# Kernel tuning notes

Hardware: AMD Instinct MI355X
Metric: run time of the kernel (lower is better)

The kernel has to match this reference:

```python
import jax, jax.numpy as jnp
import numpy as np

V, E, L, T, H, B = 8124, 1024, 24, 512, 16, 2
S = E // H
DFF = E * 8 // 3  # 2730
EPS = 1e-5
SCALE = 1.0 / np.sqrt(E)  # note: 1/sqrt(emb_dim), as in the source


def _pe():
    # sinusoidal positional encoding [T, E]
    pos = jnp.arange(T, dtype=jnp.float32)[:, None]
    div = jnp.exp(jnp.arange(0, E, 2, dtype=jnp.float32) * (-np.log(10000.0) / E))
    pe = jnp.zeros((T, E), jnp.float32)
    pe = pe.at[:, 0::2].set(jnp.sin(pos * div))
    pe = pe.at[:, 1::2].set(jnp.cos(pos * div))
    return pe


def _rms(x, g):
    # NOTE: source takes the mean over the WHOLE tensor (no dim arg)
    rms = jnp.sqrt(jnp.mean(x.astype(jnp.float32) ** 2) + EPS)
    return (x / rms * g).astype(x.dtype)


def setup_inputs() -> dict:
    key = jax.random.key(0)
    ks = jax.random.split(key, 9)
    def w(k, shape):
        return jax.random.normal(k, shape, jnp.float32) * 0.02
    return {
        "tokens": jax.random.randint(ks[0], (B, T), 0, V),
        "emb_table": w(ks[1], (V, E)),
        "Wqkv": w(ks[2], (L, E, 3 * E)), "bqkv": jnp.zeros((L, 3 * E), jnp.float32),
        "Wo": w(ks[3], (L, E, E)), "bo": jnp.zeros((L, E), jnp.float32),
        "W1": w(ks[4], (L, E, DFF)), "b1": jnp.zeros((L, DFF), jnp.float32),
        "W3": w(ks[5], (L, E, DFF)), "b3": jnp.zeros((L, DFF), jnp.float32),
        "W2": w(ks[6], (L, DFF, E)), "b2": jnp.zeros((L, E), jnp.float32),
        "g_mha": jnp.ones((L, E), jnp.float32),
        "g_ff": jnp.ones((L, E), jnp.float32),
        "g_final": jnp.ones((E,), jnp.float32),
        "Wout": w(ks[7], (E, V)), "bout": jnp.zeros((V,), jnp.float32),
    }


def reference(tokens, emb_table, Wqkv, bqkv, Wo, bo, W1, b1, W3, b3, W2, b2,
              g_mha, g_ff, g_final, Wout, bout):
    x = emb_table[tokens] + _pe()[None]  # [B,T,E]
    mask = jnp.tril(jnp.ones((T, T), bool))

    def block(x, p):
        wqkv, bq, wo, bo_, w1, b1_, w3, b3_, w2, b2_, gm, gf = p
        # --- causal MHA ---
        y = _rms(x, gm)
        qkv = (y @ wqkv + bq).reshape(B, T, H, 3, S)
        q = qkv[..., 0, :].transpose(0, 2, 1, 3)  # [B,H,T,S]
        k = qkv[..., 1, :].transpose(0, 2, 1, 3)
        v = qkv[..., 2, :].transpose(0, 2, 1, 3)
        attn = jnp.einsum('bhqd,bhkd->bhqk', q, k).astype(jnp.float32) * SCALE
        attn = jnp.where(mask, attn, -jnp.inf)
        attn = jax.nn.softmax(attn, axis=-1).astype(x.dtype)
        y = jnp.einsum('bhqk,bhkd->bhqd', attn, v)
        y = y.transpose(0, 2, 1, 3).reshape(B, T, E)
        x = x + (y @ wo + bo_)
        # --- SwiGLU FFN ---
        h = _rms(x, gf)
        u = h @ w1 + b1_
        u = u * jax.nn.sigmoid(u) * (h @ w3 + b3_)
        return x + (u @ w2 + b2_), None

    x, _ = jax.lax.scan(block, x, (Wqkv, bqkv, Wo, bo, W1, b1, W3, b3, W2, b2, g_mha, g_ff))
    return _rms(x, g_final) @ Wout + bout  # [B,T,V]
```

## Files before the change

### kernel.cpp

```cpp
#include <hip/hip_runtime.h>
#include <hip/hip_bf16.h>
#include <math.h>

#define EDIM   1024
#define TSEQ   512
#define NBATCH 2
#define NHEAD  16
#define HDIM   64
#define NLAYER 24
#define VOCAB  8124
#define DFFDIM 2730
#define DPAD   2752
#define MTOK   (NBATCH*TSEQ)
#define NELEM  (MTOK*EDIM)
#define EPSF   1e-5f
#define SCALEF (1.0f/32.0f)
#define NEGBIG (-1e30f)
#define LCONV  3088
#define ACONV  (NLAYER*LCONV)
#define HCONV  2048

typedef __bf16 bf16x8 __attribute__((ext_vector_type(8)));
typedef __bf16 bf16x4 __attribute__((ext_vector_type(4)));
typedef float  f32x4  __attribute__((ext_vector_type(4)));

#define MFMA(a, b, c) __builtin_amdgcn_mfma_f32_16x16x32_bf16((a), (b), (c), 0, 0, 0)

__device__ __forceinline__ void gl_lds16(const __bf16* g, __bf16* l) {
  __builtin_amdgcn_global_load_lds(
      (const __attribute__((address_space(1))) void*)g,
      (__attribute__((address_space(3))) void*)l, 16, 0, 0);
}
template <int N> __device__ __forceinline__ void vmwait() {
  asm volatile("s_waitcnt vmcnt(%0)" :: "n"(N) : "memory");
}
__device__ __forceinline__ void lgkm_barrier() {
  asm volatile("s_waitcnt lgkmcnt(0)" ::: "memory");
  __builtin_amdgcn_s_barrier();
}

struct ConvW {
  const float *Wqkv, *Wo, *W1, *W3, *W2w, *g_mha, *g_ff, *Wout, *g_final;
  __bf16 *qkvT, *woT, *w1T, *w3T, *w2T, *WoutT;
};

__global__ __launch_bounds__(256) void k_embed(const int* __restrict__ tok,
                                               const float* __restrict__ emb,
                                               float* __restrict__ x) {
  const int bt = blockIdx.x;
  const int t  = bt & (TSEQ - 1);
  const int tk = tok[bt];
  const float* er = emb + (size_t)tk * EDIM;
  float* xr = x + (size_t)bt * EDIM;
  for (int e = threadIdx.x * 4; e < EDIM; e += 256 * 4) {
    float4 v = *(const float4*)(er + e);
    float vv[4] = {v.x, v.y, v.z, v.w};
    float ou[4];
#pragma unroll
    for (int j = 0; j < 4; ++j) {
      int ee = e + j;
      int i2 = ee & ~1;
      float freq = expf(-(float)i2 * (9.210340371976184f / 1024.0f));
      float ang  = (float)t * freq;
      ou[j] = vv[j] + ((ee & 1) ? cosf(ang) : sinf(ang));
    }
    *(float4*)(xr + e) = make_float4(ou[0], ou[1], ou[2], ou[3]);
  }
}

__global__ __launch_bounds__(256) void k_red1f(float* __restrict__ x,
                                               const float* __restrict__ pb,
                                               int np,
                                               const float* __restrict__ bias,
                                               float* __restrict__ part,
                                               __bf16* __restrict__ ybf) {
  const int tid = threadIdx.x;
  float s = 0.f;
  const bool fold = (pb != nullptr);
  for (int i = (blockIdx.x * 256 + tid) * 4; i < NELEM; i += 256 * 256 * 4) {
    float4 v = *(const float4*)(x + i);
    if (fold) {
      for (int z = 0; z < np; ++z) {
        float4 a = *(const float4*)(pb + (size_t)z * NELEM + i);
        v.x += a.x; v.y += a.y; v.z += a.z; v.w += a.w;
      }
      float4 c = *(const float4*)(bias + (i & (EDIM - 1)));
      v.x += c.x; v.y += c.y; v.z += c.z; v.w += c.w;
      *(float4*)(x + i) = v;
    }
    bf16x4 o = {(__bf16)v.x, (__bf16)v.y, (__bf16)v.z, (__bf16)v.w};
    *(bf16x4*)(ybf + i) = o;
    s += v.x * v.x + v.y * v.y + v.z * v.z + v.w * v.w;
  }
#pragma unroll
  for (int o = 32; o > 0; o >>= 1) s += __shfl_down(s, o);
  __shared__ float sm[4];
  if ((tid & 63) == 0) sm[tid >> 6] = s;
  __syncthreads();
  if (tid == 0) part[blockIdx.x] = sm[0] + sm[1] + sm[2] + sm[3];
}

__device__ void conv_tile(const float* __restrict__ src,
                          const float* __restrict__ gk,
                          __bf16* __restrict__ dst,
                          int K, int N, int Kpad, int tk, int tn, char* smv) {
  float (*st)[65] = (float (*)[65])smv;
  const int k0 = tk << 6, n0 = tn << 6;
  const int tid = threadIdx.x;
  {
    const int r0 = tid >> 4, c4 = (tid & 15) << 2;
#pragma unroll
    for (int i = 0; i < 4; ++i) {
      const int r = r0 + i * 16;
      const int k = k0 + r;
      f32x4 v = {0.f, 0.f, 0.f, 0.f};
      if (k < K) {
        const float* sp = src + (size_t)k * N + n0 + c4;
        if (n0 + c4 + 3 < N) v = __builtin_nontemporal_load((const f32x4*)sp);
        else {
          if (n0 + c4 + 0 < N) v[0] = sp[0];
          if (n0 + c4 + 1 < N) v[1] = sp[1];
          if (n0 + c4 + 2 < N) v[2] = sp[2];
          if (n0 + c4 + 3 < N) v[3] = sp[3];
        }
        if (gk) {
          const float gv = gk[k];
          v[0] *= gv; v[1] *= gv; v[2] *= gv; v[3] *= gv;
        }
      }
      st[r][c4 + 0] = v[0]; st[r][c4 + 1] = v[1];
      st[r][c4 + 2] = v[2]; st[r][c4 + 3] = v[3];
    }
  }
  __syncthreads();
  {
    const int nl0 = tid >> 3, c8 = (tid & 7) << 3;
#pragma unroll
    for (int i = 0; i < 2; ++i) {
      const int nl = nl0 + i * 32;
      bf16x8 o = {(__bf16)st[c8 + 0][nl], (__bf16)st[c8 + 1][nl],
                  (__bf16)st[c8 + 2][nl], (__bf16)st[c8 + 3][nl],
                  (__bf16)st[c8 + 4][nl], (__bf16)st[c8 + 5][nl],
                  (__bf16)st[c8 + 6][nl], (__bf16)st[c8 + 7][nl]};
      *(bf16x8*)&dst[(size_t)(n0 + nl) * Kpad + k0 + c8] = o;
    }
  }
}

__device__ void conv_dispatch(int g, const ConvW& cw, char* sm) {
  if (g < ACONV) {
    const int l = g / LCONV;
    int b = g - l * LCONV;
    if (b < 768) {
      conv_tile(cw.Wqkv + (size_t)l * 1024 * 3072, cw.g_mha + (size_t)l * EDIM,
                cw.qkvT + (size_t)l * 3072 * 1024, 1024, 3072, 1024,
                b / 48, b % 48, sm);
    } else if (b < 1024) {
      int t = b - 768;
      conv_tile(cw.Wo + (size_t)l * 1024 * 1024, nullptr,
                cw.woT + (size_t)l * 1024 * 1024, 1024, 1024, 1024,
                t / 16, t % 16, sm);
    } else if (b < 1712) {
      int t = b - 1024;
      conv_tile(cw.W1 + (size_t)l * 1024 * DFFDIM, cw.g_ff + (size_t)l * EDIM,
                cw.w1T + (size_t)l * DPAD * 1024, 1024, DFFDIM, 1024,
                t / 43, t % 43, sm);
    } else if (b < 2400) {
      int t = b - 1712;
      conv_tile(cw.W3 + (size_t)l * 1024 * DFFDIM, cw.g_ff + (size_t)l * EDIM,
                cw.w3T + (size_t)l * DPAD * 1024, 1024, DFFDIM, 1024,
                t / 43, t % 43, sm);
    } else {
      int t = b - 2400;
      conv_tile(cw.W2w + (size_t)l * DFFDIM * 1024, nullptr,
                cw.w2T + (size_t)l * 1024 * DPAD, DFFDIM, 1024, DPAD,
                t / 16, t % 16, sm);
    }
  } else {
    const int t = g - ACONV;
    conv_tile(cw.Wout, cw.g_final, cw.WoutT, 1024, VOCAB, 1024,
              t >> 7, t & 127, sm);
  }
}

__global__ __launch_bounds__(256) void k_conv0(ConvW cw) {
  __shared__ __align__(16) char sm[16640];
  conv_dispatch(blockIdx.x, cw, sm);
}

template <int BN, int MODE, int SC>
__global__ __launch_bounds__(256) void mm(
    const __bf16* __restrict__ A,
    const __bf16* __restrict__ B0w, const __bf16* __restrict__ B1w,
    const float* __restrict__ bias0, const float* __restrict__ bias1,
    const float* __restrict__ part,
    float* __restrict__ po, __bf16* __restrict__ ob,
    __bf16* __restrict__ qout, __bf16* __restrict__ kout, __bf16* __restrict__ vout,
    int N, int lda, int ldb, int Ktot,
    int nx, int ny, int gz, ConvW cw, int convoff) {
  constexpr int DUAL = (MODE == 2) ? 2 : 1;
  constexpr int FN = BN / 32;
  constexpr int BL = (BN == 128) ? 4 : 2 * DUAL;
  constexpr int ASZ = 32768;
  constexpr int BSZ = DUAL * BN * 256;
  __shared__ __align__(16) char smem[ASZ + BSZ];
  const int bid = blockIdx.x;
  const int ncomp = nx * ny * gz;
  if (bid >= ncomp) {
    conv_dispatch(convoff + (bid - ncomp), cw, smem);
    return;
  }
  typedef __bf16 (*AsP)[8][128][8];
  typedef __bf16 (*BsP)[DUAL][8][BN][8];
  AsP As = (AsP)smem;
  BsP Bs = (BsP)(smem + ASZ);
  const int bz = bid / (nx * ny);
  const int r2 = bid - bz * nx * ny;
  const int by = r2 / nx, bx = r2 - by * nx;
  const int tid = threadIdx.x, lane = tid & 63, wave = tid >> 6;
  const int m0 = by << 7, n0 = bx * BN;
  const int wm0 = (wave >> 1) * 64, wn0 = (wave & 1) * (BN / 2);
  const int lr = lane & 15, kh = lane >> 4;

  const int ktiles = Ktot >> 6;
  const int nt0 = (ktiles + gz - 1) / gz;
  const int tbeg = bz * nt0;
  const int tend = (ktiles < tbeg + nt0) ? ktiles : (tbeg + nt0);
  const int nt = tend - tbeg;

  f32x4 acc[DUAL][4][FN];
#pragma unroll
  for (int d = 0; d < DUAL; ++d)
#pragma unroll
    for (int mi = 0; mi < 4; ++mi)
#pragma unroll
      for (int fn = 0; fn < FN; ++fn) acc[d][mi][fn] = (f32x4){0.f, 0.f, 0.f, 0.f};

  auto STAGE = [&](int buf, int t) {
    const int k0 = (tbeg + t) << 6;
#pragma unroll
    for (int i = 0; i < 4; ++i) {
      const int d = i * 256 + tid;
      gl_lds16(A + (size_t)(m0 + (d & 127)) * lda + k0 + (d >> 7) * 8,
               &As[buf][d >> 7][d & 127][0]);
    }
    if (BN == 128) {
#pragma unroll
      for (int i = 0; i < 4; ++i) {
        const int d = i * 256 + tid;
        gl_lds16(B0w + (size_t)(n0 + (d & 127)) * ldb + k0 + (d >> 7) * 8,
                 &Bs[buf][0][d >> 7][d & 127][0]);
      }
    } else {
#pragma unroll
      for (int i = 0; i < 2; ++i) {
        const int d = i * 256 + tid;
        gl_lds16(B0w + (size_t)(n0 + (d & 63)) * ldb + k0 + (d >> 6) * 8,
                 &Bs[buf][0][d >> 6][d & 63][0]);
      }
      if (DUAL == 2) {
#pragma unroll
        for (int i = 0; i < 2; ++i) {
          const int d = i * 256 + tid;
          gl_lds16(B1w + (size_t)(n0 + (d & 63)) * ldb + k0 + (d >> 6) * 8,
                   &Bs[buf][DUAL - 1][d >> 6][d & 63][0]);
        }
      }
    }
  };
  auto COMP = [&](int buf) {
#pragma unroll
    for (int ks = 0; ks < 2; ++ks) {
      const int kidx = ks * 4 + kh;
      bf16x8 af[4];
#pragma unroll
      for (int mi = 0; mi < 4; ++mi)
        af[mi] = *(const bf16x8*)&As[buf][kidx][wm0 + mi * 16 + lr][0];
#pragma unroll
      for (int d = 0; d < DUAL; ++d)
#pragma unroll
        for (int fn = 0; fn < FN; ++fn) {
          bf16x8 bfr = *(const bf16x8*)&Bs[buf][d][kidx][wn0 + fn * 16 + lr][0];
#pragma unroll
          for (int mi = 0; mi < 4; ++mi)
            acc[d][mi][fn] = MFMA(af[mi], bfr, acc[d][mi][fn]);
        }
    }
  };

  STAGE(0, 0);
  int cur = 0;
  for (int t = 0; t < nt - 1; ++t) {
    STAGE(cur ^ 1, t + 1);
    vmwait<4 + BL>();
    __builtin_amdgcn_s_barrier();
    COMP(cur);
    __builtin_amdgcn_s_barrier();
    cur ^= 1;
  }
  vmwait<0>();
  __builtin_amdgcn_s_barrier();
  COMP(cur);

  float sc = 1.0f;
  if (SC) {
    __shared__ float smr[4];
    float s = part[tid];
#pragma unroll
    for (int o = 32; o > 0; o >>= 1) s += __shfl_down(s, o);
    if ((tid & 63) == 0) smr[tid >> 6] = s;
    __syncthreads();
    sc = 1.0f / sqrtf((smr[0] + smr[1] + smr[2] + smr[3]) / (float)NELEM + EPSF);
  }

#pragma unroll
  for (int mi = 0; mi < 4; ++mi)
#pragma unroll
    for (int fn = 0; fn < FN; ++fn) {
      const int col = n0 + wn0 + fn * 16 + lr;
      if (MODE == 0) {
        const float bs = bias0[col];
        const int h = col / (3 * HDIM);
        const int rsel = (col >> 6) % 3;
        const int s2 = col & (HDIM - 1);
#pragma unroll
        for (int j = 0; j < 4; ++j) {
          const int row = m0 + wm0 + mi * 16 + (kh << 2) + j;
          const int b = row >> 9, t = row & (TSEQ - 1);
          const float v = acc[0][mi][fn][j] * sc + bs;
          if (rsel == 0)      qout[((size_t)(b * NHEAD + h) * TSEQ + t) * HDIM + s2] = (__bf16)v;
          else if (rsel == 1) kout[((size_t)(b * NHEAD + h) * TSEQ + t) * HDIM + s2] = (__bf16)v;
          else                vout[((size_t)(b * NHEAD + h) * HDIM + s2) * TSEQ + t] = (__bf16)v;
        }
      } else if (MODE == 1) {
        float* pz = po + (size_t)bz * NELEM;
#pragma unroll
        for (int j = 0; j < 4; ++j) {
          const int row = m0 + wm0 + mi * 16 + (kh << 2) + j;
          pz[(size_t)row * EDIM + col] = acc[0][mi][fn][j];
        }
      } else if (MODE == 2) {
        const bool ok = col < N;
        const float bb1 = ok ? bias0[col] : 0.f;
        const float bb3 = ok ? bias1[col] : 0.f;
#pragma unroll
        for (int j = 0; j < 4; ++j) {
          const int row = m0 + wm0 + mi * 16 + (kh << 2) + j;
          float v = 0.f;
          if (ok) {
            const float a1v = acc[0][mi][fn][j] * sc + bb1;
            const float a3v = acc[DUAL - 1][mi][fn][j] * sc + bb3;
            v = a1v * (1.0f / (1.0f + __expf(-a1v))) * a3v;
          }
          ob[(size_t)row * DPAD + col] = (__bf16)v;
        }
      } else {
        if (col < N) {
          const float bs = bias0[col];
#pragma unroll
          for (int j = 0; j < 4; ++j) {
            const int row = m0 + wm0 + mi * 16 + (kh << 2) + j;
            po[(size_t)row * N + col] = acc[0][mi][fn][j] * sc + bs;
          }
        }
      }
    }
}

__global__ __launch_bounds__(256) void k_flash(const __bf16* __restrict__ qbuf,
                                               const __bf16* __restrict__ kbuf,
                                               const __bf16* __restrict__ vbufT,
                                               __bf16* __restrict__ y2,
                                               ConvW cw, int convoff) {
  __shared__ __align__(16) char smem[41472];
  const int bid = blockIdx.x;
  if (bid >= 512) {
    conv_dispatch(convoff + (bid - 512), cw, smem);
    return;
  }
  const int qt = bid & 15, bh = bid >> 4;
  const int b = bh >> 4, h = bh & 15;
  const int m0 = qt << 5;
  const __bf16* qp = qbuf  + (size_t)bh * TSEQ * HDIM;
  const __bf16* kp = kbuf  + (size_t)bh * TSEQ * HDIM;
  const __bf16* vp = vbufT + (size_t)bh * HDIM * TSEQ;
  __bf16 (*Qs)[32][8]    = (__bf16 (*)[32][8])smem;
  __bf16 (*Ks)[8][64][8] = (__bf16 (*)[8][64][8])(smem + 4096);
  __bf16 (*Vs)[8][64][8] = (__bf16 (*)[8][64][8])(smem + 20480);
  __bf16 (*Ps)[32][8]    = (__bf16 (*)[32][8])(smem + 36864);
  float* wmaxp = (float*)(smem + 40960);
  float* wsump = wmaxp + 64;
  const int tid = threadIdx.x, lane = tid & 63, wave = tid >> 6;
  const int wm = (wave >> 1) << 4, wn = (wave & 1) << 5;
  const int lr = lane & 15, kh = lane >> 4;

  auto STAGE_KV = [&](int kt2, int buf) {
    const int n0s = kt2 << 6;
#pragma unroll
    for (int i = 0; i < 2; ++i) {
      const int d = i * 256 + tid;
      const int kb2 = d >> 6, row = d & 63;
      gl_lds16(kp + (size_t)(n0s + row) * HDIM + kb2 * 8, &Ks[buf][kb2][row][0]);
      gl_lds16(vp + (size_t)row * TSEQ + n0s + kb2 * 8, &Vs[buf][kb2][row][0]);
    }
  };

  gl_lds16(qp + (size_t)(m0 + (tid & 31)) * HDIM + (tid >> 5) * 8,
           &Qs[tid >> 5][tid & 31][0]);
  STAGE_KV(0, 0);

  float m_[4], l_[4];
#pragma unroll
  for (int j = 0; j < 4; ++j) { m_[j] = NEGBIG; l_[j] = 0.f; }
  f32x4 o0 = {0, 0, 0, 0}, o1 = {0, 0, 0, 0};

  const int ktmax = qt >> 1;
  int cur = 0;
  for (int kt = 0; kt <= ktmax; ++kt) {
    const int n0 = kt << 6;
    if (kt < ktmax) {
      STAGE_KV(kt + 1, cur ^ 1);
      vmwait<4>();
    } else {
      vmwait<0>();
    }
    __builtin_amdgcn_s_barrier();

    f32x4 s0 = {0, 0, 0, 0}, s1 = {0, 0, 0, 0};
#pragma unroll
    for (int ks = 0; ks < 2; ++ks) {
      const int kidx = ks * 4 + kh;
      bf16x8 a  = *(const bf16x8*)&Qs[kidx][wm + lr][0];
      bf16x8 b0 = *(const bf16x8*)&Ks[cur][kidx][wn + lr][0];
      bf16x8 b1 = *(const bf16x8*)&Ks[cur][kidx][wn + 16 + lr][0];
      s0 = MFMA(a, b0, s0); s1 = MFMA(a, b1, s1);
    }
    float pv0[4], pv1[4];
#pragma unroll
    for (int j = 0; j < 4; ++j) {
      const int grow = m0 + wm + (kh << 2) + j;
      float t0 = s0[j] * SCALEF; if (n0 + wn + lr > grow)      t0 = NEGBIG;
      float t1 = s1[j] * SCALEF; if (n0 + wn + 16 + lr > grow) t1 = NEGBIG;
      pv0[j] = t0; pv1[j] = t1;
      float v = fmaxf(t0, t1);
      v = fmaxf(v, __shfl_xor(v, 1)); v = fmaxf(v, __shfl_xor(v, 2));
      v = fmaxf(v, __shfl_xor(v, 4)); v = fmaxf(v, __shfl_xor(v, 8));
      wmaxp[(wave & 1) * 32 + wm + (kh << 2) + j] = v;
    }
    lgkm_barrier();

    float tmax[4]; bool need = false;
#pragma unroll
    for (int j = 0; j < 4; ++j) {
      const int rl = wm + (kh << 2) + j;
      tmax[j] = fmaxf(wmaxp[rl], wmaxp[32 + rl]);
      need |= (tmax[j] > m_[j] + 8.f);
    }
    if (__ballot(need)) {
#pragma unroll
      for (int j = 0; j < 4; ++j) {
        const float mn = fmaxf(m_[j], tmax[j]);
        const float al = __expf(m_[j] - mn);
        m_[j] = mn; l_[j] *= al; o0[j] *= al; o1[j] *= al;
      }
    }
#pragma unroll
    for (int j = 0; j < 4; ++j) {
      const float p0 = __expf(pv0[j] - m_[j]);
      const float p1 = __expf(pv1[j] - m_[j]);
      float rs = p0 + p1;
      rs += __shfl_xor(rs, 1); rs += __shfl_xor(rs, 2);
      rs += __shfl_xor(rs, 4); rs += __shfl_xor(rs, 8);
      const int rl = wm + (kh << 2) + j;
      wsump[(wave & 1) * 32 + rl] = rs;
      const int pc0 = wn + lr, pc1 = wn + 16 + lr;
      Ps[pc0 >> 3][rl][pc0 & 7] = (__bf16)p0;
      Ps[pc1 >> 3][rl][pc1 & 7] = (__bf16)p1;
    }
    lgkm_barrier();

#pragma unroll
    for (int j = 0; j < 4; ++j) {
      const int rl = wm + (kh << 2) + j;
      l_[j] += wsump[rl] + wsump[32 + rl];
    }
#pragma unroll
    for (int ks = 0; ks < 2; ++ks) {
      const int kidx = ks * 4 + kh;
      bf16x8 a  = *(const bf16x8*)&Ps[kidx][wm + lr][0];
      bf16x8 b0 = *(const bf16x8*)&Vs[cur][kidx][wn + lr][0];
      bf16x8 b1 = *(const bf16x8*)&Vs[cur][kidx][wn + 16 + lr][0];
      o0 = MFMA(a, b0, o0); o1 = MFMA(a, b1, o1);
    }
    __builtin_amdgcn_s_barrier();
    cur ^= 1;
  }

#pragma unroll
  for (int j = 0; j < 4; ++j) {
    const int row = m0 + wm + (kh << 2) + j;
    const float inv = 1.0f / l_[j];
    y2[((size_t)(b * TSEQ) + row) * EDIM + h * HDIM + wn + lr]      = (__bf16)(o0[j] * inv);
    y2[((size_t)(b * TSEQ) + row) * EDIM + h * HDIM + wn + 16 + lr] = (__bf16)(o1[j] * inv);
  }
}

extern "C" void kernel_launch(void* const* d_in, const int* in_sizes, int n_in,
                              void* d_out, int out_size, void* d_ws, size_t ws_size,
                              hipStream_t stream) {
  const int*   tokens  = (const int*)d_in[0];
  const float* emb     = (const float*)d_in[1];
  const float* Wqkv    = (const float*)d_in[2];
  const float* bqkv    = (const float*)d_in[3];
  const float* Wo      = (const float*)d_in[4];
  const float* bo      = (const float*)d_in[5];
  const float* W1      = (const float*)d_in[6];
  const float* b1      = (const float*)d_in[7];
  const float* W3      = (const float*)d_in[8];
  const float* b3      = (const float*)d_in[9];
  const float* W2w     = (const float*)d_in[10];
  const float* b2      = (const float*)d_in[11];
  const float* g_mha   = (const float*)d_in[12];
  const float* g_ff    = (const float*)d_in[13];
  const float* g_final = (const float*)d_in[14];
  const float* Wout    = (const float*)d_in[15];
  const float* bout    = (const float*)d_in[16];
  float* out = (float*)d_out;

  char* base = (char*)d_ws;
  size_t off = 0;
  auto alloc = [&](size_t bytes) { char* p = base + off; off = (off + bytes + 255) & ~(size_t)255; return p; };
  float*  x    = (float*)alloc(4u << 20);
  float*  part = (float*)alloc(2048);
  __bf16* ybf  = (__bf16*)alloc(2u << 20);
  __bf16* qbf  = (__bf16*)alloc(2u << 20);
  __bf16* kbf  = (__bf16*)alloc(2u << 20);
  __bf16* vbT  = (__bf16*)alloc(2u << 20);
  __bf16* y2bf = (__bf16*)alloc(2u << 20);
  __bf16* ubf  = (__bf16*)alloc((size_t)MTOK * DPAD * 2);
  float*  pbuf = (float*)alloc((size_t)4 * NELEM * 4);
  __bf16* WoutT = (__bf16*)alloc((size_t)8192 * 1024 * 2);
  __bf16* qkvT = (__bf16*)alloc((size_t)NLAYER * 3072 * 1024 * 2);
  __bf16* woT  = (__bf16*)alloc((size_t)NLAYER * 1024 * 1024 * 2);
  __bf16* w1T  = (__bf16*)alloc((size_t)NLAYER * DPAD * 1024 * 2);
  __bf16* w3T  = (__bf16*)alloc((size_t)NLAYER * DPAD * 1024 * 2);
  __bf16* w2T  = (__bf16*)alloc((size_t)NLAYER * 1024 * DPAD * 2);

  ConvW cw;
  cw.Wqkv = Wqkv; cw.Wo = Wo; cw.W1 = W1; cw.W3 = W3; cw.W2w = W2w;
  cw.g_mha = g_mha; cw.g_ff = g_ff; cw.Wout = Wout; cw.g_final = g_final;
  cw.qkvT = qkvT; cw.woT = woT; cw.w1T = w1T; cw.w3T = w3T; cw.w2T = w2T;
  cw.WoutT = WoutT;

  k_embed<<<MTOK, 256, 0, stream>>>(tokens, emb, x);
  k_conv0<<<LCONV, 256, 0, stream>>>(cw);
  k_red1f<<<256, 256, 0, stream>>>(x, nullptr, 0, nullptr, part, ybf);

  const float* pend_bias = nullptr;
  for (int l = 0; l < NLAYER; ++l) {
    const int co = (l + 1 < NLAYER) ? (l + 1) * LCONV : ACONV;
    const int cn = (l + 1 < NLAYER) ? 772 : 512;
    mm<64, 0, 1><<<384 + cn, 256, 0, stream>>>(
        ybf, qkvT + (size_t)l * 3072 * 1024, nullptr,
        bqkv + (size_t)l * 3 * EDIM, nullptr, part,
        nullptr, nullptr, qbf, kbf, vbT, 3072, 1024, 1024, 1024,
        48, 8, 1, cw, co);
    k_flash<<<512 + cn, 256, 0, stream>>>(qbf, kbf, vbT, y2bf, cw, co + cn);
    mm<64, 1, 0><<<512, 256, 0, stream>>>(
        y2bf, woT + (size_t)l * 1024 * 1024, nullptr,
        nullptr, nullptr, nullptr,
        pbuf, nullptr, nullptr, nullptr, nullptr, 1024, 1024, 1024, 1024,
        16, 8, 4, cw, 0);
    k_red1f<<<256, 256, 0, stream>>>(x, pbuf, 4, bo + (size_t)l * EDIM, part, ybf);
    mm<64, 2, 1><<<344 + cn, 256, 0, stream>>>(
        ybf, w1T + (size_t)l * DPAD * 1024, w3T + (size_t)l * DPAD * 1024,
        b1 + (size_t)l * DFFDIM, b3 + (size_t)l * DFFDIM, part,
        nullptr, ubf, nullptr, nullptr, nullptr, DFFDIM, 1024, 1024, 1024,
        43, 8, 1, cw, co + 2 * cn);
    mm<64, 1, 0><<<512 + cn, 256, 0, stream>>>(
        ubf, w2T + (size_t)l * 1024 * DPAD, nullptr,
        nullptr, nullptr, nullptr,
        pbuf, nullptr, nullptr, nullptr, nullptr, 1024, DPAD, DPAD, DPAD,
        16, 8, 4, cw, co + 3 * cn);
    pend_bias = b2 + (size_t)l * EDIM;
    k_red1f<<<256, 256, 0, stream>>>(x, pbuf, 4, pend_bias, part, ybf);
  }

  mm<128, 3, 1><<<512, 256, 0, stream>>>(
      ybf, WoutT, nullptr, bout, nullptr, part,
      out, nullptr, nullptr, nullptr, nullptr, VOCAB, 1024, 1024, 1024,
      64, 8, 1, cw, 0);
}
```

Before: 3.639 ms.

## Fuse split-K reduction, residual add and RMS partials into GEMM via last-block atomic

The split-K output-projection and down-projection GEMMs now count finished K-slices per output tile with an atomic counter. The last block to finish sums the partial buffers, adds bias and residual, writes fp32 x and bf16 activations, and emits a per-tile sum of squares. This removes the two standalone reduction kernel launches per layer and their extra pass over memory. The QKV GEMM also switches to 128-wide N tiles, which halves its grid. The trade-offs are more threadfence and atomic traffic, a serialized tail in the owning block, and a reliance on counter reset for correctness.

```diff
diff --git a/kernel.cpp b/kernel.cpp
--- a/kernel.cpp
+++ b/kernel.cpp
@@ -68,26 +68,13 @@
   }
 }
 
-__global__ __launch_bounds__(256) void k_red1f(float* __restrict__ x,
-                                               const float* __restrict__ pb,
-                                               int np,
-                                               const float* __restrict__ bias,
+__global__ __launch_bounds__(256) void k_red1f(const float* __restrict__ x,
                                                float* __restrict__ part,
                                                __bf16* __restrict__ ybf) {
   const int tid = threadIdx.x;
   float s = 0.f;
-  const bool fold = (pb != nullptr);
   for (int i = (blockIdx.x * 256 + tid) * 4; i < NELEM; i += 256 * 256 * 4) {
     float4 v = *(const float4*)(x + i);
-    if (fold) {
-      for (int z = 0; z < np; ++z) {
-        float4 a = *(const float4*)(pb + (size_t)z * NELEM + i);
-        v.x += a.x; v.y += a.y; v.z += a.z; v.w += a.w;
-      }
-      float4 c = *(const float4*)(bias + (i & (EDIM - 1)));
-      v.x += c.x; v.y += c.y; v.z += c.z; v.w += c.w;
-      *(float4*)(x + i) = v;
-    }
     bf16x4 o = {(__bf16)v.x, (__bf16)v.y, (__bf16)v.z, (__bf16)v.w};
     *(bf16x4*)(ybf + i) = o;
     s += v.x * v.x + v.y * v.y + v.z * v.z + v.w * v.w;
@@ -193,9 +180,10 @@
     const __bf16* __restrict__ A,
     const __bf16* __restrict__ B0w, const __bf16* __restrict__ B1w,
     const float* __restrict__ bias0, const float* __restrict__ bias1,
-    const float* __restrict__ part,
+    const float* __restrict__ part, int pcount,
     float* __restrict__ po, __bf16* __restrict__ ob,
     __bf16* __restrict__ qout, __bf16* __restrict__ kout, __bf16* __restrict__ vout,
+    float* __restrict__ xres, float* __restrict__ part_out, int* __restrict__ cnt,
     int N, int lda, int ldb, int Ktot,
     int nx, int ny, int gz, ConvW cw, int convoff) {
   constexpr int DUAL = (MODE == 2) ? 2 : 1;
@@ -305,7 +293,7 @@
   float sc = 1.0f;
   if (SC) {
     __shared__ float smr[4];
-    float s = part[tid];
+    float s = (tid < pcount) ? part[tid] : 0.f;
 #pragma unroll
     for (int o = 32; o > 0; o >>= 1) s += __shfl_down(s, o);
     if ((tid & 63) == 0) smr[tid >> 6] = s;
@@ -365,6 +353,45 @@
         }
       }
     }
+
+  if (MODE == 1) {
+    const int tile = by * nx + bx;
+    __threadfence();
+    __syncthreads();
+    __shared__ int own;
+    if (tid == 0) {
+      const int old = atomicAdd(&cnt[tile], 1);
+      own = (old == gz - 1) ? 1 : 0;
+      if (own) atomicExch(&cnt[tile], 0);
+    }
+    __syncthreads();
+    if (!own) return;
+    __threadfence();
+    float ssum = 0.f;
+#pragma unroll
+    for (int i = 0; i < 8; ++i) {
+      const int idx = i * 256 + tid;
+      const int row = m0 + (idx >> 4);
+      const int c4  = n0 + ((idx & 15) << 2);
+      f32x4 v = *(const f32x4*)(xres + (size_t)row * EDIM + c4);
+      for (int z = 0; z < gz; ++z) {
+        f32x4 p = *(const f32x4*)(po + (size_t)z * NELEM + (size_t)row * EDIM + c4);
+        v[0] += p[0]; v[1] += p[1]; v[2] += p[2]; v[3] += p[3];
+      }
+      const f32x4 bb = *(const f32x4*)(bias0 + c4);
+      v[0] += bb[0]; v[1] += bb[1]; v[2] += bb[2]; v[3] += bb[3];
+      *(f32x4*)(xres + (size_t)row * EDIM + c4) = v;
+      bf16x4 o = {(__bf16)v[0], (__bf16)v[1], (__bf16)v[2], (__bf16)v[3]};
+      *(bf16x4*)(ob + (size_t)row * EDIM + c4) = o;
+      ssum += v[0] * v[0] + v[1] * v[1] + v[2] * v[2] + v[3] * v[3];
+    }
+#pragma unroll
+    for (int o = 32; o > 0; o >>= 1) ssum += __shfl_down(ssum, o);
+    __shared__ float smf[4];
+    if ((tid & 63) == 0) smf[tid >> 6] = ssum;
+    __syncthreads();
+    if (tid == 0) part_out[tile] = smf[0] + smf[1] + smf[2] + smf[3];
+  }
 }
 
 __global__ __launch_bounds__(256) void k_flash(const __bf16* __restrict__ qbuf,
@@ -532,6 +559,7 @@
   auto alloc = [&](size_t bytes) { char* p = base + off; off = (off + bytes + 255) & ~(size_t)255; return p; };
   float*  x    = (float*)alloc(4u << 20);
   float*  part = (float*)alloc(2048);
+  int*    cnt  = (int*)alloc(1024);
   __bf16* ybf  = (__bf16*)alloc(2u << 20);
   __bf16* qbf  = (__bf16*)alloc(2u << 20);
   __bf16* kbf  = (__bf16*)alloc(2u << 20);
@@ -552,42 +580,40 @@
   cw.qkvT = qkvT; cw.woT = woT; cw.w1T = w1T; cw.w3T = w3T; cw.w2T = w2T;
   cw.WoutT = WoutT;
 
+  hipMemsetAsync(cnt, 0, 1024, stream);
   k_embed<<<MTOK, 256, 0, stream>>>(tokens, emb, x);
   k_conv0<<<LCONV, 256, 0, stream>>>(cw);
-  k_red1f<<<256, 256, 0, stream>>>(x, nullptr, 0, nullptr, part, ybf);
-
-  const float* pend_bias = nullptr;
+  k_red1f<<<256, 256, 0, stream>>>(x, part, ybf);
+
   for (int l = 0; l < NLAYER; ++l) {
     const int co = (l + 1 < NLAYER) ? (l + 1) * LCONV : ACONV;
     const int cn = (l + 1 < NLAYER) ? 772 : 512;
-    mm<64, 0, 1><<<384 + cn, 256, 0, stream>>>(
+    const int pc = (l == 0) ? 256 : 128;
+    mm<128, 0, 1><<<192 + cn, 256, 0, stream>>>(
         ybf, qkvT + (size_t)l * 3072 * 1024, nullptr,
-        bqkv + (size_t)l * 3 * EDIM, nullptr, part,
-        nullptr, nullptr, qbf, kbf, vbT, 3072, 1024, 1024, 1024,
-        48, 8, 1, cw, co);
+        bqkv + (size_t)l * 3 * EDIM, nullptr, part, pc,
+        nullptr, nullptr, qbf, kbf, vbT, nullptr, nullptr, nullptr,
+        3072, 1024, 1024, 1024, 24, 8, 1, cw, co);
     k_flash<<<512 + cn, 256, 0, stream>>>(qbf, kbf, vbT, y2bf, cw, co + cn);
     mm<64, 1, 0><<<512, 256, 0, stream>>>(
         y2bf, woT + (size_t)l * 1024 * 1024, nullptr,
-        nullptr, nullptr, nullptr,
-        pbuf, nullptr, nullptr, nullptr, nullptr, 1024, 1024, 1024, 1024,
-        16, 8, 4, cw, 0);
-    k_red1f<<<256, 256, 0, stream>>>(x, pbuf, 4, bo + (size_t)l * EDIM, part, ybf);
+        bo + (size_t)l * EDIM, nullptr, nullptr, 0,
+        pbuf, ybf, nullptr, nullptr, nullptr, x, part, cnt,
+        1024, 1024, 1024, 1024, 16, 8, 4, cw, 0);
     mm<64, 2, 1><<<344 + cn, 256, 0, stream>>>(
         ybf, w1T + (size_t)l * DPAD * 1024, w3T + (size_t)l * DPAD * 1024,
-        b1 + (size_t)l * DFFDIM, b3 + (size_t)l * DFFDIM, part,
-        nullptr, ubf, nullptr, nullptr, nullptr, DFFDIM, 1024, 1024, 1024,
-        43, 8, 1, cw, co + 2 * cn);
+        b1 + (size_t)l * DFFDIM, b3 + (size_t)l * DFFDIM, part, 128,
+        nullptr, ubf, nullptr, nullptr, nullptr, nullptr, nullptr, nullptr,
+        DFFDIM, 1024, 1024, 1024, 43, 8, 1, cw, co + 2 * cn);
     mm<64, 1, 0><<<512 + cn, 256, 0, stream>>>(
         ubf, w2T + (size_t)l * 1024 * DPAD, nullptr,
-        nullptr, nullptr, nullptr,
-        pbuf, nullptr, nullptr, nullptr, nullptr, 1024, DPAD, DPAD, DPAD,
-        16, 8, 4, cw, co + 3 * cn);
-    pend_bias = b2 + (size_t)l * EDIM;
-    k_red1f<<<256, 256, 0, stream>>>(x, pbuf, 4, pend_bias, part, ybf);
+        b2 + (size_t)l * EDIM, nullptr, nullptr, 0,
+        pbuf, ybf, nullptr, nullptr, nullptr, x, part, cnt,
+        1024, DPAD, DPAD, DPAD, 16, 8, 4, cw, co + 3 * cn);
   }
 
   mm<128, 3, 1><<<512, 256, 0, stream>>>(
-      ybf, WoutT, nullptr, bout, nullptr, part,
-      out, nullptr, nullptr, nullptr, nullptr, VOCAB, 1024, 1024, 1024,
-      64, 8, 1, cw, 0);
-}
+      ybf, WoutT, nullptr, bout, nullptr, part, 128,
+      out, nullptr, nullptr, nullptr, nullptr, nullptr, nullptr, nullptr,
+      VOCAB, 1024, 1024, 1024, 64, 8, 1, cw, 0);
+}
```

Result: slower. 7.332 ms (+101.4%).
